# Optimization experiments

Measured on AMD Instinct MI355X. Metric: run time of the kernel, lower is better.

Reference implementation:

```python
import jax, jax.numpy as jnp
import numpy as np

N, E, K, IN, OUT = 20000, 320000, 5, 256, 128
NAN_FRAC = 0.3


def setup_inputs() -> dict:
    key = jax.random.key(0)
    ks = jax.random.split(key, 8)
    x = jax.random.normal(ks[0], (N, IN), dtype=jnp.float32)
    nan_mask = jax.random.uniform(ks[1], (N, IN)) < NAN_FRAC
    x = jnp.where(nan_mask, jnp.nan, x)  # missing features as NaN
    edge_index = jax.random.randint(ks[2], (2, E), 0, N, dtype=jnp.int64)
    logp = jax.nn.log_softmax(jax.random.normal(ks[3], (K,), dtype=jnp.float32))
    means = jax.random.normal(ks[4], (K, IN), dtype=jnp.float32)
    logvars = jax.random.normal(ks[5], (K, IN), dtype=jnp.float32) * 0.1
    xav = 1.414 * np.sqrt(6.0 / (IN + OUT))
    weight = jax.random.uniform(ks[6], (IN, OUT), dtype=jnp.float32, minval=-xav, maxval=xav)
    bias = jnp.zeros((OUT,), dtype=jnp.float32)
    return {"x": x, "edge_index": edge_index, "logp": logp, "means": means,
            "logvars": logvars, "weight": weight, "bias": bias}


def _ex_relu(mu, sigma):
    # E[relu(X)] for X ~ N(mu, sigma); sigma is the variance
    sigma_s = jnp.where(sigma == 0, 1e-10, sigma)
    ss = jnp.sqrt(sigma_s)
    w = mu / ss
    nr = ss * (jnp.exp(-0.5 * w * w) / np.sqrt(2 * np.pi)
               + 0.5 * w * (1.0 + jax.lax.erf(w / np.sqrt(2))))
    return jnp.where(sigma == 0, jnp.maximum(mu, 0.0), nr)


def _gcn_norm(edge_index, num_nodes):
    # add self-loops, symmetric D^-1/2 A D^-1/2 normalization
    row = jnp.concatenate([edge_index[0], jnp.arange(num_nodes, dtype=edge_index.dtype)])
    col = jnp.concatenate([edge_index[1], jnp.arange(num_nodes, dtype=edge_index.dtype)])
    ones = jnp.ones(row.shape[0], dtype=jnp.float32)
    deg = jax.ops.segment_sum(ones, row, num_segments=num_nodes)
    dinv = jnp.where(deg > 0, jax.lax.rsqrt(deg), 0.0)
    wn = dinv[row] * dinv[col]
    return row, col, wn


def reference(x, edge_index, logp, means, logvars, weight, bias):
    n = x.shape[0]
    dim = x.shape[1]
    row, col, wn = _gcn_norm(edge_index, n)
    wn2 = wn * wn  # adj2 = adj * adj (elementwise on sparse values)

    isnan = jnp.isnan(x)                                       # [N, IN]
    variances = jnp.exp(logvars)                               # [K, IN]
    mean_mat = jnp.where(isnan[None], means[:, None, :], x[None])      # [K, N, IN]
    var_mat = jnp.where(isnan[None], variances[:, None, :], 0.0)       # [K, N, IN]

    transform_x = jnp.einsum('kni,io->kno', mean_mat, weight) + bias   # [K, N, OUT]
    transform_covs = jnp.einsum('kni,io->kno', var_mat, weight * weight)

    def spmm(vals, X):  # segment-sum SpMM: out[r] += vals_e * X[c]
        return jax.ops.segment_sum(X[col] * vals[:, None], row, num_segments=n)

    conv_x = jax.vmap(lambda X: spmm(wn, X))(transform_x)      # [K, N, OUT]
    conv_covs = jax.vmap(lambda X: spmm(wn2, X))(transform_covs)

    expected_x = _ex_relu(conv_x, conv_covs)                   # [K, N, OUT]

    # GMM responsibilities per node
    log_n = (-0.5 * jnp.sum((mean_mat - means[:, None, :]) ** 2 / variances[:, None, :], axis=2)
             - 0.5 * dim * np.log(2 * np.pi) - 0.5 * jnp.sum(logvars))  # [K, N]
    gamma = jax.nn.softmax(logp[:, None] + log_n, axis=0)      # [K, N]

    return jnp.sum(expected_x * gamma[:, :, None], axis=0)     # [N, OUT]
```

## Files before the change

### kernel.cpp

```cpp
#include <hip/hip_runtime.h>
#include <stdint.h>

#define N_NODES 20000
#define N_EDGES 320000
#define K_MIX 5
#define IN_F 256
#define OUT_F 128
#define NT 11
#define TC (NT * OUT_F)
#define BSTRIDE 96
#define MT_TILES ((N_NODES + 127) / 128)
#define GEMM_WGS (MT_TILES * NT)

typedef __attribute__((ext_vector_type(8))) short short8;
typedef __attribute__((ext_vector_type(4))) float floatx4;

__device__ __forceinline__ float bf2f(unsigned int u) {
  union { unsigned int i; float f; } v;
  v.i = (u & 0xffffu) << 16;
  return v.f;
}
__device__ __forceinline__ unsigned short f2bf(float f) {
  union { float f; unsigned int i; } v;
  v.f = f;
  unsigned int x = v.i;
  unsigned int r = (x + 0x7fffu + ((x >> 16) & 1u)) >> 16;
  return (unsigned short)r;
}

__device__ __forceinline__ float exrelu(float mu, float sig) {
  if (sig < 1e-30f) return fmaxf(mu, 0.f);
  float ss = sqrtf(sig);
  float w = mu / ss;
  float e = __expf(-0.5f * w * w);
  float axv = fabsf(w) * 0.70710678118654752f;
  float t = 1.f / (1.f + 0.3275911f * axv);
  float poly = t * (0.254829592f +
              t * (-0.284496736f +
              t * (1.421413741f +
              t * (-1.453152027f + t * 1.061405429f))));
  float erfv = 1.f - poly * e;
  erfv = copysignf(erfv, w);
  return ss * (e * 0.3989422804014327f + 0.5f * w * (1.f + erfv));
}

__device__ __forceinline__ void gll16(const void* g, void* l) {
  __builtin_amdgcn_global_load_lds(
      (const __attribute__((address_space(1))) void*)g,
      (__attribute__((address_space(3))) void*)l, 16, 0, 0);
}

__global__ void k_scatter(const int* __restrict__ row, const int* __restrict__ col,
                          int* __restrict__ cursor, int* __restrict__ bucket) {
  int t = blockIdx.x * 256 + threadIdx.x;
  if (t < N_EDGES) {
    int r = row[t];
    int p = atomicAdd(&cursor[r], 1);
    bucket[r * BSTRIDE + p] = col[t];
  }
}

__global__ void k_buildB(const float* __restrict__ W, const float* __restrict__ means,
                         const float* __restrict__ logvars, unsigned short* __restrict__ Bt) {
  int idx = blockIdx.x * 256 + threadIdx.x;
  int j = idx >> 15;
  int rem = idx & 32767;
  int n = rem >> 8;
  int kk = rem & 255;
  float wv = W[kk * OUT_F + n];
  float val;
  if (j == 0) val = wv;
  else if (j <= 5) val = means[(j - 1) * IN_F + kk] * wv;
  else val = expf(logvars[(j - 6) * IN_F + kk]) * wv * wv;
  Bt[idx] = f2bf(val);
}

__global__ void k_prepx(const float* __restrict__ x, const float* __restrict__ logp,
                        const float* __restrict__ means, const float* __restrict__ logvars,
                        unsigned short* __restrict__ X0, unsigned char* __restrict__ Xn,
                        float* __restrict__ gamma) {
  __shared__ float s_mean[K_MIX * IN_F];
  __shared__ float s_rv[K_MIX * IN_F];
  int t = threadIdx.x;
  for (int j = t; j < K_MIX * IN_F; j += 256) {
    s_mean[j] = means[j];
    s_rv[j] = expf(-logvars[j]);
  }
  __syncthreads();
  int node = blockIdx.x * 4 + (t >> 6);
  if (node >= N_NODES) return;
  int lane = t & 63;
  float4 xv = *(const float4*)(x + (size_t)node * IN_F + 4 * lane);
  float xf[4] = {xv.x, xv.y, xv.z, xv.w};
  float gsum[K_MIX] = {0, 0, 0, 0, 0};
  ushort4 o;
  unsigned short* op = (unsigned short*)&o;
  unsigned int nb = 0;
#pragma unroll
  for (int j = 0; j < 4; j++) {
    bool nn = (xf[j] != xf[j]);
    op[j] = nn ? (unsigned short)0 : f2bf(xf[j]);
    if (nn) nb |= (1u << j);
    if (!nn) {
      int fi = 4 * lane + j;
#pragma unroll
      for (int k = 0; k < K_MIX; k++) {
        float d = xf[j] - s_mean[k * IN_F + fi];
        gsum[k] += d * d * s_rv[k * IN_F + fi];
      }
    }
  }
  *(ushort4*)(X0 + (size_t)node * IN_F + 4 * lane) = o;
  Xn[node * 64 + lane] = (unsigned char)nb;
#pragma unroll
  for (int k = 0; k < K_MIX; k++)
    for (int off = 32; off; off >>= 1) gsum[k] += __shfl_xor(gsum[k], off, 64);
  if (lane == 0) {
    float lg[K_MIX], mx = -1e30f;
#pragma unroll
    for (int k = 0; k < K_MIX; k++) {
      lg[k] = logp[k] - 0.5f * gsum[k];
      mx = fmaxf(mx, lg[k]);
    }
    float se = 0.f;
#pragma unroll
    for (int k = 0; k < K_MIX; k++) { lg[k] = expf(lg[k] - mx); se += lg[k]; }
    float inv = 1.f / se;
#pragma unroll
    for (int k = 0; k < K_MIX; k++) gamma[node * K_MIX + k] = lg[k] * inv;
  }
}

__global__ __launch_bounds__(256) void k_spmm(const unsigned short* __restrict__ X0,
                       const unsigned char* __restrict__ Xn,
                       const int* __restrict__ deg, const int* __restrict__ bucket,
                       unsigned short* __restrict__ G, float* __restrict__ sArr) {
  int wvid = threadIdx.x >> 6;
  int lane = threadIdx.x & 63;
  int node = __builtin_amdgcn_readfirstlane(blockIdx.x * 4 + wvid);
  int fo = 4 * lane;
  float ax[4] = {0, 0, 0, 0}, am[4] = {0, 0, 0, 0}, am2[4] = {0, 0, 0, 0};
  float ssum = 0.f;
  int dv = __builtin_amdgcn_readfirstlane(deg[node]);
  float ds = rsqrtf((float)(dv + 1));
  float ws = ds * ds;
  int st = node * BSTRIDE;
  int total = dv + 1;
  ushort4 zero4 = {0, 0, 0, 0};
  ushort4 B0 = zero4, B1 = zero4, B2 = zero4, B3 = zero4,
          B4 = zero4, B5 = zero4, B6 = zero4, B7 = zero4;
  unsigned int M0 = 0, M1 = 0, M2 = 0, M3 = 0, M4 = 0, M5 = 0, M6 = 0, M7 = 0;
  float W0 = 0.f, W1 = 0.f, W2 = 0.f, W3 = 0.f,
        W4 = 0.f, W5 = 0.f, W6 = 0.f, W7 = 0.f;
  B0 = *(const ushort4*)(X0 + (size_t)node * IN_F + fo);
  M0 = Xn[node * 64 + lane];
  W0 = ws;
#define PFILL(S)                                                      \
  if (S < total) {                                                    \
    int c = bucket[st + (S - 1)];                                     \
    W##S = ds * rsqrtf((float)(deg[c] + 1));                          \
    B##S = *(const ushort4*)(X0 + (size_t)c * IN_F + fo);             \
    M##S = Xn[c * 64 + lane];                                         \
  }
  PFILL(1) PFILL(2) PFILL(3) PFILL(4) PFILL(5) PFILL(6) PFILL(7)
#undef PFILL

#define STEP(S)                                                       \
  if (W##S != 0.f) {                                                  \
    float wvv = W##S, wv2 = wvv * wvv;                                \
    ssum += wvv;                                                      \
    const unsigned short* xp = (const unsigned short*)&B##S;          \
    unsigned int mb = M##S;                                           \
    _Pragma("unroll")                                                 \
    for (int j = 0; j < 4; j++) {                                     \
      float nf = (float)((mb >> j) & 1u);                             \
      ax[j] = fmaf(wvv, bf2f(xp[j]), ax[j]);                          \
      am[j] = fmaf(wvv, nf, am[j]);                                   \
      am2[j] = fmaf(wv2, nf, am2[j]);                                 \
    }                                                                 \
  }                                                                   \
  if (base + 8 + S < total) {                                         \
    int c = bucket[st + base + 7 + S];                                \
    W##S = ds * rsqrtf((float)(deg[c] + 1));                          \
    B##S = *(const ushort4*)(X0 + (size_t)c * IN_F + fo);             \
    M##S = Xn[c * 64 + lane];                                         \
  } else {                                                            \
    W##S = 0.f;                                                       \
  }

  for (int base = 0; base < total; base += 8) {
    STEP(0) STEP(1) STEP(2) STEP(3) STEP(4) STEP(5) STEP(6) STEP(7)
  }
#undef STEP

  ushort4 o;
  o.x = f2bf(ax[0]); o.y = f2bf(ax[1]); o.z = f2bf(ax[2]); o.w = f2bf(ax[3]);
  *(ushort4*)(G + node * 768 + fo) = o;
  o.x = f2bf(am[0]); o.y = f2bf(am[1]); o.z = f2bf(am[2]); o.w = f2bf(am[3]);
  *(ushort4*)(G + node * 768 + 256 + fo) = o;
  o.x = f2bf(am2[0]); o.y = f2bf(am2[1]); o.z = f2bf(am2[2]); o.w = f2bf(am2[3]);
  *(ushort4*)(G + node * 768 + 512 + fo) = o;
  if (lane == 0) sArr[node] = ssum;
}

__global__ __launch_bounds__(256) void k_gemm(const unsigned short* __restrict__ G,
                                              const unsigned short* __restrict__ Bt,
                                              unsigned short* __restrict__ T) {
  __shared__ __align__(16) char Als[128 * 64 * 2];
  __shared__ __align__(16) char Bls[128 * 64 * 2];
  int linear = blockIdx.x;
  const int q = GEMM_WGS / 8, r = GEMM_WGS % 8;
  int xcd = linear & 7, ixd = linear >> 3;
  int orig = (xcd < r ? xcd * (q + 1) : r * (q + 1) + (xcd - r) * q) + ixd;
  int mt = orig / NT, jt = orig - mt * NT;
  int aoff = (jt == 0) ? 0 : (jt <= 5 ? 256 : 512);
  int t = threadIdx.x, w = t >> 6, lane = t & 63;
  int wr = w >> 1, wc = w & 1;
  int quad = lane >> 4, l16 = lane & 15;
  const unsigned short* Bp = Bt + (size_t)jt * 32768;

  floatx4 acc[4][4];
  floatx4 z = {0.f, 0.f, 0.f, 0.f};
#pragma unroll
  for (int mi = 0; mi < 4; mi++)
#pragma unroll
    for (int ni = 0; ni < 4; ni++) acc[mi][ni] = z;

  for (int k0 = 0; k0 < 256; k0 += 64) {
    __syncthreads();
#pragma unroll
    for (int i = 0; i < 4; i++) {
      int rr = i * 32 + w * 8 + (lane >> 3);
      int c = (lane & 7) ^ (rr & 7);
      int gr = mt * 128 + rr;
      if (gr >= N_NODES) gr = N_NODES - 1;
      gll16(G + (size_t)gr * 768 + aoff + k0 + c * 8, Als + i * 4096 + w * 1024);
      gll16(Bp + (size_t)rr * 256 + k0 + c * 8, Bls + i * 4096 + w * 1024);
    }
    __syncthreads();
#pragma unroll
    for (int ks = 0; ks < 2; ks++) {
      int cc = ks * 4 + quad;
      short8 a[4], b[4];
#pragma unroll
      for (int mi = 0; mi < 4; mi++) {
        int rr = wr * 64 + mi * 16 + l16;
        a[mi] = *(const short8*)(Als + rr * 128 + (cc ^ (rr & 7)) * 16);
      }
#pragma unroll
      for (int ni = 0; ni < 4; ni++) {
        int rr = wc * 64 + ni * 16 + l16;
        b[ni] = *(const short8*)(Bls + rr * 128 + (cc ^ (rr & 7)) * 16);
      }
#pragma unroll
      for (int mi = 0; mi < 4; mi++)
#pragma unroll
        for (int ni = 0; ni < 4; ni++)
          acc[mi][ni] = __builtin_amdgcn_mfma_f32_16x16x32_bf16(a[mi], b[ni], acc[mi][ni], 0, 0, 0);
    }
  }
#pragma unroll
  for (int mi = 0; mi < 4; mi++)
#pragma unroll
    for (int ni = 0; ni < 4; ni++) {
      int gc = jt * 128 + wc * 64 + ni * 16 + l16;
#pragma unroll
      for (int reg = 0; reg < 4; reg++) {
        int gr = mt * 128 + wr * 64 + mi * 16 + quad * 4 + reg;
        if (gr < N_NODES) T[(size_t)gr * TC + gc] = f2bf(acc[mi][ni][reg]);
      }
    }
}

__global__ void k_final(const unsigned short* __restrict__ T, const float* __restrict__ gamma,
                        const float* __restrict__ sArr, const float* __restrict__ bias,
                        float* __restrict__ out) {
  int t = threadIdx.x;
  int node = blockIdx.x * 4 + (t >> 6);
  if (node >= N_NODES) return;
  int lane = t & 63;
  int o0 = 2 * lane;
  float g[K_MIX];
#pragma unroll
  for (int k = 0; k < K_MIX; k++) g[k] = gamma[node * K_MIX + k];
  float sv = sArr[node];
  float b0 = bias[o0], b1 = bias[o0 + 1];
  const unsigned short* Tr = T + (size_t)node * TC;
  unsigned int c0u = *(const unsigned int*)(Tr + o0);
  float cx0 = bf2f(c0u), cx1 = bf2f(c0u >> 16);
  float a0 = 0.f, a1 = 0.f;
#pragma unroll
  for (int k = 0; k < K_MIX; k++) {
    unsigned int tm = *(const unsigned int*)(Tr + 128 * (1 + k) + o0);
    unsigned int tv = *(const unsigned int*)(Tr + 128 * (6 + k) + o0);
    float mu0 = cx0 + bf2f(tm) + b0 * sv;
    float mu1 = cx1 + bf2f(tm >> 16) + b1 * sv;
    a0 += g[k] * exrelu(mu0, bf2f(tv));
    a1 += g[k] * exrelu(mu1, bf2f(tv >> 16));
  }
  float2 ov = {a0, a1};
  *(float2*)(out + (size_t)node * OUT_F + o0) = ov;
}

extern "C" void kernel_launch(void* const* d_in, const int* in_sizes, int n_in,
                              void* d_out, int out_size, void* d_ws, size_t ws_size,
                              hipStream_t stream) {
  const float* x = (const float*)d_in[0];
  const int* ei = (const int*)d_in[1];
  const float* logp = (const float*)d_in[2];
  const float* means = (const float*)d_in[3];
  const float* lvar = (const float*)d_in[4];
  const float* W = (const float*)d_in[5];
  const float* bias = (const float*)d_in[6];
  float* out = (float*)d_out;
  const int* row = ei;
  const int* col = ei + N_EDGES;

  char* p = (char*)d_ws;
  auto alloc = [&](size_t bytes) -> char* {
    char* q = p;
    p += (bytes + 255) & ~((size_t)255);
    return q;
  };
  int* cursor = (int*)alloc(N_NODES * 4);
  int* bucket = (int*)alloc((size_t)N_NODES * BSTRIDE * 4);
  float* gamma = (float*)alloc((size_t)N_NODES * K_MIX * 4);
  float* sArr = (float*)alloc(N_NODES * 4);
  unsigned short* Bt = (unsigned short*)alloc((size_t)NT * 128 * 256 * 2);
  unsigned short* X0 = (unsigned short*)alloc((size_t)N_NODES * IN_F * 2);
  unsigned char* Xn = (unsigned char*)alloc((size_t)N_NODES * 64);
  unsigned short* G = (unsigned short*)alloc((size_t)N_NODES * 768 * 2);
  unsigned short* T = (unsigned short*)alloc((size_t)N_NODES * TC * 2);

  hipMemsetAsync(cursor, 0, N_NODES * 4, stream);
  k_scatter<<<(N_EDGES + 255) / 256, 256, 0, stream>>>(row, col, cursor, bucket);
  k_buildB<<<(NT * 128 * 256) / 256, 256, 0, stream>>>(W, means, lvar, Bt);
  k_prepx<<<N_NODES / 4, 256, 0, stream>>>(x, logp, means, lvar, X0, Xn, gamma);
  k_spmm<<<N_NODES / 4, 256, 0, stream>>>(X0, Xn, cursor, bucket, G, sArr);
  k_gemm<<<GEMM_WGS, 256, 0, stream>>>(G, Bt, T);
  k_final<<<N_NODES / 4, 256, 0, stream>>>(T, gamma, sArr, bias, out);
}
```

Measured before the change: 207.6 us.

## Encode NaN mask in bf16 X0 and preload edge list per wave via readlane

Drops the separate per-node NaN bitmask array and instead stores a bf16 NaN sentinel in X0, so the SpMM tests NaN directly from the gathered features and skips one gather stream per neighbor. The SpMM now loads up to 63 neighbor indices and normalization weights cooperatively across the wave once, computes the weight sum with a wave reduction, and broadcasts each neighbor with readlane instead of issuing serial scalar loads of bucket and deg per edge. Neighbors beyond 63 fall back to a slow serial loop. This reduces memory traffic and dependent-load latency in the gather at the cost of extra readlane instructions and isnan selects.

```diff
diff --git a/kernel.cpp b/kernel.cpp
--- a/kernel.cpp
+++ b/kernel.cpp
@@ -50,6 +50,10 @@
       (__attribute__((address_space(3))) void*)l, 16, 0, 0);
 }
 
+__device__ __forceinline__ float readlane_f(float v, int l) {
+  return __int_as_float(__builtin_amdgcn_readlane(__float_as_int(v), l));
+}
+
 __global__ void k_scatter(const int* __restrict__ row, const int* __restrict__ col,
                           int* __restrict__ cursor, int* __restrict__ bucket) {
   int t = blockIdx.x * 256 + threadIdx.x;
@@ -77,8 +81,7 @@
 
 __global__ void k_prepx(const float* __restrict__ x, const float* __restrict__ logp,
                         const float* __restrict__ means, const float* __restrict__ logvars,
-                        unsigned short* __restrict__ X0, unsigned char* __restrict__ Xn,
-                        float* __restrict__ gamma) {
+                        unsigned short* __restrict__ X0, float* __restrict__ gamma) {
   __shared__ float s_mean[K_MIX * IN_F];
   __shared__ float s_rv[K_MIX * IN_F];
   int t = threadIdx.x;
@@ -95,12 +98,10 @@
   float gsum[K_MIX] = {0, 0, 0, 0, 0};
   ushort4 o;
   unsigned short* op = (unsigned short*)&o;
-  unsigned int nb = 0;
 #pragma unroll
   for (int j = 0; j < 4; j++) {
     bool nn = (xf[j] != xf[j]);
-    op[j] = nn ? (unsigned short)0 : f2bf(xf[j]);
-    if (nn) nb |= (1u << j);
+    op[j] = nn ? (unsigned short)0x7FC0 : f2bf(xf[j]);
     if (!nn) {
       int fi = 4 * lane + j;
 #pragma unroll
@@ -111,7 +112,6 @@
     }
   }
   *(ushort4*)(X0 + (size_t)node * IN_F + 4 * lane) = o;
-  Xn[node * 64 + lane] = (unsigned char)nb;
 #pragma unroll
   for (int k = 0; k < K_MIX; k++)
     for (int off = 32; off; off >>= 1) gsum[k] += __shfl_xor(gsum[k], off, 64);
@@ -132,66 +132,100 @@
 }
 
 __global__ __launch_bounds__(256) void k_spmm(const unsigned short* __restrict__ X0,
-                       const unsigned char* __restrict__ Xn,
                        const int* __restrict__ deg, const int* __restrict__ bucket,
                        unsigned short* __restrict__ G, float* __restrict__ sArr) {
   int wvid = threadIdx.x >> 6;
   int lane = threadIdx.x & 63;
   int node = __builtin_amdgcn_readfirstlane(blockIdx.x * 4 + wvid);
   int fo = 4 * lane;
-  float ax[4] = {0, 0, 0, 0}, am[4] = {0, 0, 0, 0}, am2[4] = {0, 0, 0, 0};
-  float ssum = 0.f;
   int dv = __builtin_amdgcn_readfirstlane(deg[node]);
   float ds = rsqrtf((float)(dv + 1));
   float ws = ds * ds;
-  int st = node * BSTRIDE;
-  int total = dv + 1;
+
+  int c_l = 0;
+  float w_l = 0.f;
+  if (lane < dv) {
+    int c = bucket[node * BSTRIDE + lane];
+    c_l = c;
+    w_l = ds * rsqrtf((float)(deg[c] + 1));
+  }
+  float ssum = (lane == 0) ? ws : 0.f;
+  ssum += w_l;
+#pragma unroll
+  for (int off = 32; off; off >>= 1) ssum += __shfl_xor(ssum, off, 64);
+
+  float ax[4] = {0, 0, 0, 0}, am[4] = {0, 0, 0, 0}, am2[4] = {0, 0, 0, 0};
+
+  {
+    ushort4 Bs = *(const ushort4*)(X0 + (size_t)node * IN_F + fo);
+    const unsigned short* xp = (const unsigned short*)&Bs;
+#pragma unroll
+    for (int j = 0; j < 4; j++) {
+      float xf = bf2f(xp[j]);
+      bool nn = (xf != xf);
+      ax[j] = fmaf(ws, nn ? 0.f : xf, ax[j]);
+      am[j] += nn ? ws : 0.f;
+      am2[j] += nn ? ws * ws : 0.f;
+    }
+  }
+
+  int te = (dv < 63) ? dv : 63;
   ushort4 zero4 = {0, 0, 0, 0};
   ushort4 B0 = zero4, B1 = zero4, B2 = zero4, B3 = zero4,
           B4 = zero4, B5 = zero4, B6 = zero4, B7 = zero4;
-  unsigned int M0 = 0, M1 = 0, M2 = 0, M3 = 0, M4 = 0, M5 = 0, M6 = 0, M7 = 0;
   float W0 = 0.f, W1 = 0.f, W2 = 0.f, W3 = 0.f,
         W4 = 0.f, W5 = 0.f, W6 = 0.f, W7 = 0.f;
-  B0 = *(const ushort4*)(X0 + (size_t)node * IN_F + fo);
-  M0 = Xn[node * 64 + lane];
-  W0 = ws;
 #define PFILL(S)                                                      \
-  if (S < total) {                                                    \
-    int c = bucket[st + (S - 1)];                                     \
-    W##S = ds * rsqrtf((float)(deg[c] + 1));                          \
+  if (S < te) {                                                       \
+    int c = __builtin_amdgcn_readlane(c_l, S);                        \
+    W##S = readlane_f(w_l, S);                                        \
     B##S = *(const ushort4*)(X0 + (size_t)c * IN_F + fo);             \
-    M##S = Xn[c * 64 + lane];                                         \
-  }
-  PFILL(1) PFILL(2) PFILL(3) PFILL(4) PFILL(5) PFILL(6) PFILL(7)
+  }
+  PFILL(0) PFILL(1) PFILL(2) PFILL(3) PFILL(4) PFILL(5) PFILL(6) PFILL(7)
 #undef PFILL
 
 #define STEP(S)                                                       \
-  if (W##S != 0.f) {                                                  \
+  {                                                                   \
     float wvv = W##S, wv2 = wvv * wvv;                                \
-    ssum += wvv;                                                      \
     const unsigned short* xp = (const unsigned short*)&B##S;          \
-    unsigned int mb = M##S;                                           \
     _Pragma("unroll")                                                 \
     for (int j = 0; j < 4; j++) {                                     \
-      float nf = (float)((mb >> j) & 1u);                             \
-      ax[j] = fmaf(wvv, bf2f(xp[j]), ax[j]);                          \
-      am[j] = fmaf(wvv, nf, am[j]);                                   \
-      am2[j] = fmaf(wv2, nf, am2[j]);                                 \
+      float xf = bf2f(xp[j]);                                         \
+      bool nn = (xf != xf);                                           \
+      ax[j] = fmaf(wvv, nn ? 0.f : xf, ax[j]);                        \
+      am[j] += nn ? wvv : 0.f;                                        \
+      am2[j] += nn ? wv2 : 0.f;                                       \
     }                                                                 \
   }                                                                   \
-  if (base + 8 + S < total) {                                         \
-    int c = bucket[st + base + 7 + S];                                \
-    W##S = ds * rsqrtf((float)(deg[c] + 1));                          \
+  if (base + 8 + S < te) {                                            \
+    int idx = base + 8 + S;                                           \
+    int c = __builtin_amdgcn_readlane(c_l, idx);                      \
+    W##S = readlane_f(w_l, idx);                                      \
     B##S = *(const ushort4*)(X0 + (size_t)c * IN_F + fo);             \
-    M##S = Xn[c * 64 + lane];                                         \
   } else {                                                            \
     W##S = 0.f;                                                       \
   }
 
-  for (int base = 0; base < total; base += 8) {
+  for (int base = 0; base < te; base += 8) {
     STEP(0) STEP(1) STEP(2) STEP(3) STEP(4) STEP(5) STEP(6) STEP(7)
   }
 #undef STEP
+
+  for (int i = 63; i < dv; ++i) {
+    int c = bucket[node * BSTRIDE + i];
+    float wvv = ds * rsqrtf((float)(deg[c] + 1));
+    float wv2 = wvv * wvv;
+    ushort4 Bt4 = *(const ushort4*)(X0 + (size_t)c * IN_F + fo);
+    const unsigned short* xp = (const unsigned short*)&Bt4;
+#pragma unroll
+    for (int j = 0; j < 4; j++) {
+      float xf = bf2f(xp[j]);
+      bool nn = (xf != xf);
+      ax[j] = fmaf(wvv, nn ? 0.f : xf, ax[j]);
+      am[j] += nn ? wvv : 0.f;
+      am2[j] += nn ? wv2 : 0.f;
+    }
+  }
 
   ushort4 o;
   o.x = f2bf(ax[0]); o.y = f2bf(ax[1]); o.z = f2bf(ax[2]); o.w = f2bf(ax[3]);
@@ -328,15 +362,14 @@
   float* sArr = (float*)alloc(N_NODES * 4);
   unsigned short* Bt = (unsigned short*)alloc((size_t)NT * 128 * 256 * 2);
   unsigned short* X0 = (unsigned short*)alloc((size_t)N_NODES * IN_F * 2);
-  unsigned char* Xn = (unsigned char*)alloc((size_t)N_NODES * 64);
   unsigned short* G = (unsigned short*)alloc((size_t)N_NODES * 768 * 2);
   unsigned short* T = (unsigned short*)alloc((size_t)N_NODES * TC * 2);
 
   hipMemsetAsync(cursor, 0, N_NODES * 4, stream);
   k_scatter<<<(N_EDGES + 255) / 256, 256, 0, stream>>>(row, col, cursor, bucket);
   k_buildB<<<(NT * 128 * 256) / 256, 256, 0, stream>>>(W, means, lvar, Bt);
-  k_prepx<<<N_NODES / 4, 256, 0, stream>>>(x, logp, means, lvar, X0, Xn, gamma);
-  k_spmm<<<N_NODES / 4, 256, 0, stream>>>(X0, Xn, cursor, bucket, G, sArr);
+  k_prepx<<<N_NODES / 4, 256, 0, stream>>>(x, logp, means, lvar, X0, gamma);
+  k_spmm<<<N_NODES / 4, 256, 0, stream>>>(X0, cursor, bucket, G, sArr);
   k_gemm<<<GEMM_WGS, 256, 0, stream>>>(G, Bt, T);
   k_final<<<N_NODES / 4, 256, 0, stream>>>(T, gamma, sArr, bias, out);
 }
```

Result: faster. 198.6 us (median of 2 runs) (-4.3%).
